# Optimization experiments

Hardware: AMD Instinct MI355X
Metric: run time of the kernel (lower is better)

The kernel has to match this reference:

```python
import jax, jax.numpy as jnp
import numpy as np

HID = 1024
HEADS = 16
HEAD_DIM = HID // HEADS
FFN = 4096
EPS = 1e-5


def setup_inputs() -> dict:
    key = jax.random.key(0)
    ks = jax.random.split(key, 12)
    s = lambda k, shape, fan_in: jax.random.normal(k, shape, jnp.float32) * (fan_in ** -0.5)
    return {
        "hidden_states": jax.random.normal(ks[0], (2, 2048, HID), jnp.float32),
        "Wq": s(ks[1], (HID, HID), HID),
        "Wk": s(ks[2], (HID, HID), HID),
        "Wv": s(ks[3], (HID, HID), HID),
        "Wo": s(ks[4], (HID, HID), HID),
        "W1": s(ks[5], (HID, FFN), HID),
        "b1": jnp.zeros((FFN,), jnp.float32),
        "W2": s(ks[6], (FFN, HID), FFN),
        "b2": jnp.zeros((HID,), jnp.float32),
        "ln1_scale": jnp.ones((HID,), jnp.float32),
        "ln1_shift": jnp.zeros((HID,), jnp.float32),
        "ln2_scale": jnp.ones((HID,), jnp.float32),
        "ln2_shift": jnp.zeros((HID,), jnp.float32),
    }


def _layer_norm(x, scale, shift):
    mean = jnp.mean(x, axis=-1, keepdims=True)
    var = jnp.var(x, axis=-1, keepdims=True)  # biased, matches unbiased=False
    return (x - mean) * jax.lax.rsqrt(var + EPS) * scale + shift


def _forward(hidden_states, Wq, Wk, Wv, Wo, W1, b1, W2, b2,
             ln1_scale, ln1_shift, ln2_scale, ln2_shift):
    bsz, seq_len, _ = hidden_states.shape
    residual = hidden_states
    x = _layer_norm(hidden_states, ln1_scale, ln1_shift)

    # q/k/v projections -> [b, h, s, d]
    def proj(W):
        return (x @ W).reshape(bsz, seq_len, HEADS, HEAD_DIM).transpose(0, 2, 1, 3)
    q, k, v = proj(Wq), proj(Wk), proj(Wv)

    scores = jnp.einsum("bhqd,bhkd->bhqk", q, k)
    causal = jnp.triu(jnp.ones((seq_len, seq_len), bool), k=1)
    scores = jnp.where(causal, -jnp.inf, scores) / (HEAD_DIM ** 0.5)
    attn = jax.nn.softmax(scores, axis=-1)  # dropout is identity in eval
    out = jnp.einsum("bhqk,bhkd->bhqd", attn, v)
    out = out.transpose(0, 2, 1, 3).reshape(bsz, seq_len, HID)
    hidden_states = residual + out @ Wo

    residual = hidden_states
    y = _layer_norm(hidden_states, ln2_scale, ln2_shift)
    y = jax.nn.gelu(y @ W1 + b1, approximate=False) @ W2 + b2  # torch nn.GELU default = exact erf
    return residual + y


def reference(hidden_states, Wq, Wk, Wv, Wo, W1, b1, W2, b2,
              ln1_scale, ln1_shift, ln2_scale, ln2_shift):
    return _forward(hidden_states, Wq, Wk, Wv, Wo, W1, b1, W2, b2,
                    ln1_scale, ln1_shift, ln2_scale, ln2_shift)
```

## Files before the change

kernel.cpp:

```cpp
#include <hip/hip_runtime.h>
#include <math.h>

using bf16x8 = __attribute__((ext_vector_type(8))) short;
using f32x4  = __attribute__((ext_vector_type(4))) float;

struct __align__(8) us4 { unsigned short x, y, z, w; };
struct __align__(8) u32x2 { unsigned int x, y; };

__device__ __forceinline__ unsigned short f2b(float f) {
  union { float f; unsigned u; } v; v.f = f;
  unsigned r = v.u + 0x7FFFu + ((v.u >> 16) & 1u);
  return (unsigned short)(r >> 16);
}
__device__ __forceinline__ unsigned int cvt_pk_bf16(float lo, float hi) {
  unsigned int d;
  asm("v_cvt_pk_bf16_f32 %0, %1, %2" : "=v"(d) : "v"(lo), "v"(hi));
  return d;
}

#define GLDS(g, l) __builtin_amdgcn_global_load_lds(                        \
    (const __attribute__((address_space(1))) void*)(g),                    \
    (__attribute__((address_space(3))) void*)(l), 16, 0, 0)

__global__ void __launch_bounds__(256) prep_kernel(
    const float* __restrict__ hs, const float* __restrict__ ln1s,
    const float* __restrict__ ln1b, unsigned short* __restrict__ xb,
    const float* __restrict__ Wq, const float* __restrict__ Wk,
    const float* __restrict__ Wv, const float* __restrict__ Wo,
    const float* __restrict__ W1, const float* __restrict__ W2,
    unsigned short* __restrict__ wqkvT, unsigned short* __restrict__ woT,
    unsigned short* __restrict__ w1T, unsigned short* __restrict__ w2T) {
  const int id = blockIdx.x;
  const int t = threadIdx.x;
  __shared__ float tile[32][33];
  __shared__ float red[8];

  if (id < 4096) {
    const int row = id;
    const float4 v = ((const float4*)(hs + (size_t)row * 1024))[t];
    float s  = v.x + v.y + v.z + v.w;
    float s2 = v.x * v.x + v.y * v.y + v.z * v.z + v.w * v.w;
#pragma unroll
    for (int off = 32; off; off >>= 1) {
      s  += __shfl_xor(s,  off);
      s2 += __shfl_xor(s2, off);
    }
    const int w = t >> 6, lane = t & 63;
    if (!lane) { red[w] = s; red[4 + w] = s2; }
    __syncthreads();
    s  = red[0] + red[1] + red[2] + red[3];
    s2 = red[4] + red[5] + red[6] + red[7];
    const float mean = s * (1.0f / 1024.0f);
    const float var  = s2 * (1.0f / 1024.0f) - mean * mean;
    const float rstd = rsqrtf(var + 1e-5f);
    const float4 sc = ((const float4*)ln1s)[t];
    const float4 sh = ((const float4*)ln1b)[t];
    us4 o;
    o.x = f2b((v.x - mean) * rstd * sc.x + sh.x);
    o.y = f2b((v.y - mean) * rstd * sc.y + sh.y);
    o.z = f2b((v.z - mean) * rstd * sc.z + sh.z);
    o.w = f2b((v.w - mean) * rstd * sc.w + sh.w);
    ((us4*)(xb + (size_t)row * 1024))[t] = o;
    return;
  }

  const float* src; unsigned short* dst; int K, N, n0, k0;
  if (id < 8192) {
    const int which = (id - 4096) >> 10, local = (id - 4096) & 1023;
    src = (which == 0) ? Wq : (which == 1) ? Wk : (which == 2) ? Wv : Wo;
    dst = (which == 3) ? woT : wqkvT + (size_t)which * 1048576;
    K = 1024; N = 1024;
    n0 = (local & 31) * 32; k0 = (local >> 5) * 32;
  } else if (id < 12288) {
    const int local = id - 8192;
    src = W1; dst = w1T; K = 1024; N = 4096;
    n0 = (local & 127) * 32; k0 = (local >> 7) * 32;
  } else {
    const int local = id - 12288;
    src = W2; dst = w2T; K = 4096; N = 1024;
    n0 = (local & 31) * 32; k0 = (local >> 5) * 32;
  }
  const int tx = t & 31, ty = t >> 5;
#pragma unroll
  for (int i = 0; i < 32; i += 8)
    tile[ty + i][tx] = src[(size_t)(k0 + ty + i) * N + n0 + tx];
  __syncthreads();
#pragma unroll
  for (int i = 0; i < 32; i += 8)
    dst[(size_t)(n0 + ty + i) * K + k0 + tx] = f2b(tile[tx][ty + i]);
}

__global__ void __launch_bounds__(256) ln_kernel(
    const float* __restrict__ in, const float* __restrict__ scale,
    const float* __restrict__ shift, unsigned short* __restrict__ out) {
  const int row = blockIdx.x, t = threadIdx.x;
  const float4 v = ((const float4*)(in + (size_t)row * 1024))[t];
  float s  = v.x + v.y + v.z + v.w;
  float s2 = v.x * v.x + v.y * v.y + v.z * v.z + v.w * v.w;
#pragma unroll
  for (int off = 32; off; off >>= 1) {
    s  += __shfl_xor(s,  off);
    s2 += __shfl_xor(s2, off);
  }
  __shared__ float red[8];
  const int w = t >> 6, lane = t & 63;
  if (!lane) { red[w] = s; red[4 + w] = s2; }
  __syncthreads();
  s  = red[0] + red[1] + red[2] + red[3];
  s2 = red[4] + red[5] + red[6] + red[7];
  const float mean = s * (1.0f / 1024.0f);
  const float var  = s2 * (1.0f / 1024.0f) - mean * mean;
  const float rstd = rsqrtf(var + 1e-5f);
  const float4 sc = ((const float4*)scale)[t];
  const float4 sh = ((const float4*)shift)[t];
  us4 o;
  o.x = f2b((v.x - mean) * rstd * sc.x + sh.x);
  o.y = f2b((v.y - mean) * rstd * sc.y + sh.y);
  o.z = f2b((v.z - mean) * rstd * sc.z + sh.z);
  o.w = f2b((v.w - mean) * rstd * sc.w + sh.w);
  ((us4*)(out + (size_t)row * 1024))[t] = o;
}

template <int MODE>
__global__ void __launch_bounds__(512, 2) gemm256(
    const unsigned short* __restrict__ A, const unsigned short* __restrict__ B,
    int K, int N, unsigned short* __restrict__ outb,
    const float* __restrict__ bias, unsigned short* __restrict__ vt) {
  __shared__ unsigned short lA[2][256 * 64];
  __shared__ unsigned short lB[2][256 * 64];
  const int t = threadIdx.x, lane = t & 63;
  const int w = t >> 6, wm = w >> 2, wn = w & 3;
  const int r16 = lane & 15, g = lane >> 4;
  const int m0 = blockIdx.x * 256, n0 = blockIdx.y * 256;

  const unsigned short* aSrc[4];
  const unsigned short* bSrc[4];
#pragma unroll
  for (int p = 0; p < 4; ++p) {
    const int ci = t + p * 512, r = ci >> 3, cs = ci & 7;
    aSrc[p] = A + (size_t)(m0 + r) * K + (cs ^ (r & 7)) * 8;
    bSrc[p] = B + (size_t)(n0 + r) * K + (cs ^ (r & 7)) * 8;
  }
  int aOff[8][2], bOff[4][2];
#pragma unroll
  for (int i = 0; i < 8; ++i)
#pragma unroll
    for (int ks = 0; ks < 2; ++ks) {
      const int m = wm * 128 + i * 16 + r16, kb = ks * 4 + g;
      aOff[i][ks] = ((m << 3) + (kb ^ (m & 7))) << 3;
    }
#pragma unroll
  for (int j = 0; j < 4; ++j)
#pragma unroll
    for (int ks = 0; ks < 2; ++ks) {
      const int n = wn * 64 + j * 16 + r16, kb = ks * 4 + g;
      bOff[j][ks] = ((n << 3) + (kb ^ (n & 7))) << 3;
    }

  auto stage = [&](int buf, int kt) {
    const int off = kt * 64;
#pragma unroll
    for (int p = 0; p < 4; ++p) {
      GLDS(aSrc[p] + off, &lA[buf][(t + p * 512) * 8]);
      GLDS(bSrc[p] + off, &lB[buf][(t + p * 512) * 8]);
    }
  };

  f32x4 acc[8][4] = {};
  const int nkt = K >> 6;
  stage(0, 0);
  for (int kt = 0; kt < nkt; ++kt) {
    const int cur = kt & 1;
    if (kt + 1 < nkt) {
      stage(cur ^ 1, kt + 1);
      asm volatile("s_waitcnt vmcnt(8)" ::: "memory");
    } else {
      asm volatile("s_waitcnt vmcnt(0)" ::: "memory");
    }
    __builtin_amdgcn_s_barrier();
    __builtin_amdgcn_sched_barrier(0);
    const unsigned short* bA = lA[cur];
    const unsigned short* bB = lB[cur];
#pragma unroll
    for (int ks = 0; ks < 2; ++ks) {
      bf16x8 af[8], bfr[4];
#pragma unroll
      for (int i = 0; i < 8; ++i) af[i] = *(const bf16x8*)&bA[aOff[i][ks]];
#pragma unroll
      for (int j = 0; j < 4; ++j) bfr[j] = *(const bf16x8*)&bB[bOff[j][ks]];
      __builtin_amdgcn_s_setprio(1);
#pragma unroll
      for (int i = 0; i < 8; ++i)
#pragma unroll
        for (int j = 0; j < 4; ++j)
          acc[i][j] = __builtin_amdgcn_mfma_f32_16x16x32_bf16(
              af[i], bfr[j], acc[i][j], 0, 0, 0);
      __builtin_amdgcn_s_setprio(0);
    }
    __builtin_amdgcn_sched_barrier(0);
    __builtin_amdgcn_s_barrier();
  }

  float bj[4];
  if constexpr (MODE == 2) {
#pragma unroll
    for (int j = 0; j < 4; ++j) bj[j] = bias[n0 + wn * 64 + j * 16 + r16];
  }
#pragma unroll
  for (int i = 0; i < 8; ++i) {
    const int row0 = m0 + wm * 128 + i * 16 + g * 4;
#pragma unroll
    for (int j = 0; j < 4; ++j) {
      const int colb = n0 + wn * 64 + j * 16;
      const int col = colb + r16;
      if constexpr (MODE == 0) {
        if (colb < 2048) {
#pragma unroll
          for (int r = 0; r < 4; ++r)
            outb[(size_t)(row0 + r) * 2048 + col] = f2b(acc[i][j][r]);
        } else {
          const int b = row0 >> 11, s0 = row0 & 2047;
          us4 pk;
          pk.x = f2b(acc[i][j][0]); pk.y = f2b(acc[i][j][1]);
          pk.z = f2b(acc[i][j][2]); pk.w = f2b(acc[i][j][3]);
          *(us4*)&vt[((size_t)b * 1024 + (col - 2048)) * 2048 + s0] = pk;
        }
      } else {
#pragma unroll
        for (int r = 0; r < 4; ++r) {
          const float x = acc[i][j][r] + bj[j];
          const float u = x * (0.7978845608028654f + 0.03567740814f * x * x);
          const float e = __builtin_amdgcn_exp2f(u * 2.885390081777927f);
          const float th = 1.0f - 2.0f * __builtin_amdgcn_rcpf(e + 1.0f);
          outb[(size_t)(row0 + r) * N + col] = f2b(0.5f * x * (1.0f + th));
        }
      }
    }
  }
}

template <int MODE, int BM>
__global__ void __launch_bounds__(256) gemm_bt(
    const unsigned short* __restrict__ A, const unsigned short* __restrict__ B,
    int K, int N,
    float* __restrict__ outf, const float* __restrict__ bias,
    const float* __restrict__ resid) {
  constexpr int WN = (BM == 128) ? 2 : 4;
  constexpr int NJ = 128 / (16 * WN);
  constexpr int ACH = BM / 32;
  __shared__ unsigned short lA[2][BM * 64];
  __shared__ unsigned short lB[2][128 * 64];
  const int t = threadIdx.x, lane = t & 63;
  const int w = t >> 6, wm = w / WN, wn = w % WN;
  const int r16 = lane & 15, g = lane >> 4;
  const int m0 = blockIdx.x * BM, n0 = blockIdx.y * 128;

  const unsigned short* aSrc[ACH];
  const unsigned short* bSrc[4];
#pragma unroll
  for (int p = 0; p < ACH; ++p) {
    const int ci = t + p * 256, m = ci >> 3, cs = ci & 7;
    aSrc[p] = A + (size_t)(m0 + m) * K + (cs ^ (m & 7)) * 8;
  }
#pragma unroll
  for (int p = 0; p < 4; ++p) {
    const int ci = t + p * 256, m = ci >> 3, cs = ci & 7;
    bSrc[p] = B + (size_t)(n0 + m) * K + (cs ^ (m & 7)) * 8;
  }

  int aOff[4][2], bOff[NJ][2];
#pragma unroll
  for (int i = 0; i < 4; ++i)
#pragma unroll
    for (int ks = 0; ks < 2; ++ks) {
      const int m = wm * 64 + i * 16 + r16, kb = ks * 4 + g;
      aOff[i][ks] = ((m << 3) + (kb ^ (m & 7))) << 3;
    }
#pragma unroll
  for (int j = 0; j < NJ; ++j)
#pragma unroll
    for (int ks = 0; ks < 2; ++ks) {
      const int n = wn * (16 * NJ) + j * 16 + r16, kb = ks * 4 + g;
      bOff[j][ks] = ((n << 3) + (kb ^ (n & 7))) << 3;
    }

  auto stage = [&](int buf, int kt) {
    const int off = kt * 64;
#pragma unroll
    for (int p = 0; p < ACH; ++p)
      GLDS(aSrc[p] + off, &lA[buf][(t + p * 256) * 8]);
#pragma unroll
    for (int p = 0; p < 4; ++p)
      GLDS(bSrc[p] + off, &lB[buf][(t + p * 256) * 8]);
  };

  f32x4 acc[4][NJ] = {};
  const int nkt = K >> 6;
  stage(0, 0);
  for (int kt = 0; kt < nkt; ++kt) {
    const int cur = kt & 1;
    if (kt + 1 < nkt) {
      stage(cur ^ 1, kt + 1);
      if constexpr (ACH == 2)
        asm volatile("s_waitcnt vmcnt(6)" ::: "memory");
      else
        asm volatile("s_waitcnt vmcnt(8)" ::: "memory");
    } else {
      asm volatile("s_waitcnt vmcnt(0)" ::: "memory");
    }
    __builtin_amdgcn_s_barrier();
    __builtin_amdgcn_sched_barrier(0);
    const unsigned short* bA = lA[cur];
    const unsigned short* bB = lB[cur];
#pragma unroll
    for (int ks = 0; ks < 2; ++ks) {
      bf16x8 af[4], bfr[NJ];
#pragma unroll
      for (int i = 0; i < 4; ++i) af[i] = *(const bf16x8*)&bA[aOff[i][ks]];
#pragma unroll
      for (int j = 0; j < NJ; ++j) bfr[j] = *(const bf16x8*)&bB[bOff[j][ks]];
      __builtin_amdgcn_s_setprio(1);
#pragma unroll
      for (int i = 0; i < 4; ++i)
#pragma unroll
        for (int j = 0; j < NJ; ++j)
          acc[i][j] = __builtin_amdgcn_mfma_f32_16x16x32_bf16(
              af[i], bfr[j], acc[i][j], 0, 0, 0);
      __builtin_amdgcn_s_setprio(0);
    }
    __builtin_amdgcn_sched_barrier(0);
    __builtin_amdgcn_s_barrier();
  }

  float bj[NJ];
  if constexpr (MODE == 3) {
#pragma unroll
    for (int j = 0; j < NJ; ++j)
      bj[j] = bias[n0 + wn * (16 * NJ) + j * 16 + r16];
  }
#pragma unroll
  for (int i = 0; i < 4; ++i) {
    const int row0 = m0 + wm * 64 + i * 16 + g * 4;
#pragma unroll
    for (int j = 0; j < NJ; ++j) {
      const int col = n0 + wn * (16 * NJ) + j * 16 + r16;
      if constexpr (MODE == 1) {
#pragma unroll
        for (int r = 0; r < 4; ++r) {
          const size_t idx = (size_t)(row0 + r) * N + col;
          outf[idx] = acc[i][j][r] + resid[idx];
        }
      } else {
#pragma unroll
        for (int r = 0; r < 4; ++r) {
          const size_t idx = (size_t)(row0 + r) * N + col;
          outf[idx] = acc[i][j][r] + bj[j] + resid[idx];
        }
      }
    }
  }
}

__global__ void __launch_bounds__(256) attn_kernel(
    const unsigned short* __restrict__ qk, const unsigned short* __restrict__ vt,
    unsigned short* __restrict__ obuf) {
  const int j = blockIdx.x, h = blockIdx.y, bb = blockIdx.z;
  const int t = threadIdx.x, lane = t & 63, w = t >> 6;
  const int r16 = lane & 15, g = lane >> 4;
  __shared__ unsigned short lK[2][64 * 64];
  __shared__ unsigned short lV[2][64 * 64];
  __shared__ unsigned short lP[4][16 * 64];

  const int qtA = j, qtB = 31 - j;
  const int ktmax = qtB;
  const int qrowA = qtA * 64 + w * 16 + r16;
  const int qrowB = qtB * 64 + w * 16 + r16;
  const float CE = 0.18033688011112042f;

  bf16x8 qfA[2], qfB[2];
  {
    const unsigned short* qa = qk + (size_t)(bb * 2048 + qrowA) * 2048 + h * 64;
    qfA[0] = *(const bf16x8*)(qa + g * 8);
    qfA[1] = *(const bf16x8*)(qa + 32 + g * 8);
    const unsigned short* qb = qk + (size_t)(bb * 2048 + qrowB) * 2048 + h * 64;
    qfB[0] = *(const bf16x8*)(qb + g * 8);
    qfB[1] = *(const bf16x8*)(qb + 32 + g * 8);
  }

  f32x4 accA[4] = {}, accB[4] = {};
  float mA = -3.0e38f, lA_ = 0.0f, mB = -3.0e38f, lB_ = 0.0f;

  auto stage = [&](int buf, int kt) {
    const int k0 = kt * 64;
#pragma unroll
    for (int p = 0; p < 2; ++p) {
      const int ci = t + p * 256;
      const int r = ci >> 3, cs = ci & 7;
      const int cb = cs ^ (r & 7);
      GLDS(qk + (size_t)(bb * 2048 + k0 + r) * 2048 + 1024 + h * 64 + cb * 8,
           &lK[buf][ci * 8]);
      GLDS(vt + ((size_t)bb * 1024 + h * 64 + r) * 2048 + k0 + cb * 8,
           &lV[buf][ci * 8]);
    }
  };

  const int pswz = (r16 & 7) << 3;

  auto flash_step = [&](const bf16x8* qf, f32x4* accO, float& mrun,
                        float& lrun, int qrow, bool diag, int k0, int cur) {
    f32x4 s[4] = {};
    __builtin_amdgcn_s_setprio(1);
#pragma unroll
    for (int ks = 0; ks < 2; ++ks)
#pragma unroll
      for (int mt = 0; mt < 4; ++mt) {
        const int r = mt * 16 + r16, db = ks * 4 + g;
        const bf16x8 kf =
            *(const bf16x8*)&lK[cur][((r << 3) + (db ^ (r & 7))) << 3];
        s[mt] = __builtin_amdgcn_mfma_f32_16x16x32_bf16(kf, qf[ks], s[mt],
                                                        0, 0, 0);
      }
    __builtin_amdgcn_s_setprio(0);
    if (diag) {
#pragma unroll
      for (int mt = 0; mt < 4; ++mt)
#pragma unroll
        for (int r = 0; r < 4; ++r)
          if (k0 + mt * 16 + g * 4 + r > qrow) s[mt][r] = -3.0e38f;
    }
    float tmax = -3.0e38f;
#pragma unroll
    for (int mt = 0; mt < 4; ++mt)
#pragma unroll
      for (int r = 0; r < 4; ++r) tmax = fmaxf(tmax, s[mt][r]);
    tmax = fmaxf(tmax, __shfl_xor(tmax, 16));
    tmax = fmaxf(tmax, __shfl_xor(tmax, 32));
    if (!__all(tmax <= mrun + 44.0f)) {
      const float mnew = fmaxf(mrun, tmax);
      const float fac = __builtin_amdgcn_exp2f((mrun - mnew) * CE);
      lrun *= fac;
      float fr[4];
#pragma unroll
      for (int r = 0; r < 4; ++r) fr[r] = __shfl(fac, g * 4 + r);
#pragma unroll
      for (int nb = 0; nb < 4; ++nb)
#pragma unroll
        for (int r = 0; r < 4; ++r) accO[nb][r] *= fr[r];
      mrun = mnew;
    }
    float pv[4][4];
    float tsum = 0.0f;
#pragma unroll
    for (int mt = 0; mt < 4; ++mt)
#pragma unroll
      for (int r = 0; r < 4; ++r) {
        pv[mt][r] = __builtin_amdgcn_exp2f((s[mt][r] - mrun) * CE);
        tsum += pv[mt][r];
      }
    tsum += __shfl_xor(tsum, 16);
    tsum += __shfl_xor(tsum, 32);
    lrun += tsum;
#pragma unroll
    for (int mt = 0; mt < 4; ++mt) {
      u32x2 pk;
      pk.x = cvt_pk_bf16(pv[mt][0], pv[mt][1]);
      pk.y = cvt_pk_bf16(pv[mt][2], pv[mt][3]);
      *(u32x2*)&lP[w][r16 * 64 + ((mt * 16 + g * 4) ^ pswz)] = pk;
    }
    __builtin_amdgcn_s_setprio(1);
#pragma unroll
    for (int ks = 0; ks < 2; ++ks) {
      const bf16x8 pa =
          *(const bf16x8*)&lP[w][r16 * 64 + ((ks * 32 + g * 8) ^ pswz)];
#pragma unroll
      for (int nb = 0; nb < 4; ++nb) {
        const int d = nb * 16 + r16, kb = ks * 4 + g;
        const bf16x8 vf =
            *(const bf16x8*)&lV[cur][((d << 3) + (kb ^ (d & 7))) << 3];
        accO[nb] = __builtin_amdgcn_mfma_f32_16x16x32_bf16(pa, vf, accO[nb],
                                                           0, 0, 0);
      }
    }
    __builtin_amdgcn_s_setprio(0);
  };

  stage(0, 0);
  __syncthreads();
  int cur = 0;
  for (int kt = 0; kt <= ktmax; ++kt) {
    if (kt < ktmax) stage(cur ^ 1, kt + 1);
    flash_step(qfB, accB, mB, lB_, qrowB, kt == qtB, kt * 64, cur);
    if (kt <= qtA)
      flash_step(qfA, accA, mA, lA_, qrowA, kt == qtA, kt * 64, cur);
    __syncthreads();
    cur ^= 1;
  }

  auto epilogue = [&](const f32x4* accO, float lrun, int q0) {
    const float li = 1.0f / lrun;
    float lr_[4];
#pragma unroll
    for (int r = 0; r < 4; ++r) lr_[r] = __shfl(li, g * 4 + r);
#pragma unroll
    for (int nb = 0; nb < 4; ++nb)
#pragma unroll
      for (int r = 0; r < 4; ++r) {
        const int row = bb * 2048 + q0 + w * 16 + g * 4 + r;
        const int col = h * 64 + nb * 16 + r16;
        obuf[(size_t)row * 1024 + col] = f2b(accO[nb][r] * lr_[r]);
      }
  };
  epilogue(accA, lA_, qtA * 64);
  epilogue(accB, lB_, qtB * 64);
}

extern "C" void kernel_launch(void* const* d_in, const int* in_sizes, int n_in,
                              void* d_out, int out_size, void* d_ws,
                              size_t ws_size, hipStream_t stream) {
  const float* hs   = (const float*)d_in[0];
  const float* Wq   = (const float*)d_in[1];
  const float* Wk   = (const float*)d_in[2];
  const float* Wv   = (const float*)d_in[3];
  const float* Wo   = (const float*)d_in[4];
  const float* W1   = (const float*)d_in[5];
  const float* b1   = (const float*)d_in[6];
  const float* W2   = (const float*)d_in[7];
  const float* b2   = (const float*)d_in[8];
  const float* ln1s = (const float*)d_in[9];
  const float* ln1b = (const float*)d_in[10];
  const float* ln2s = (const float*)d_in[11];
  const float* ln2b = (const float*)d_in[12];
  float* out = (float*)d_out;

  char* ws = (char*)d_ws;
  unsigned short* wqkvT = (unsigned short*)(ws + 0);
  unsigned short* woT   = (unsigned short*)(ws + 6291456);
  unsigned short* w1T   = (unsigned short*)(ws + 8388608);
  unsigned short* w2T   = (unsigned short*)(ws + 16777216);
  float*          hid   = (float*)(ws + 25165824);
  unsigned short* xb    = (unsigned short*)(ws + 41943040);
  char*           big   = ws + 50331648;
  unsigned short* qkb   = (unsigned short*)(big);
  unsigned short* vtb   = (unsigned short*)(big + 16777216);
  unsigned short* ob    = (unsigned short*)(big + 25165824);
  unsigned short* h1    = (unsigned short*)(big);

  prep_kernel<<<16384, 256, 0, stream>>>(hs, ln1s, ln1b, xb,
                                         Wq, Wk, Wv, Wo, W1, W2,
                                         wqkvT, woT, w1T, w2T);
  gemm256<0><<<dim3(16, 12), 512, 0, stream>>>(xb, wqkvT, 1024, 3072,
                                               qkb, nullptr, vtb);
  attn_kernel<<<dim3(16, 16, 2), 256, 0, stream>>>(qkb, vtb, ob);
  gemm_bt<1, 64><<<dim3(64, 8), 256, 0, stream>>>(ob, woT, 1024, 1024,
                                                  hid, nullptr, hs);
  ln_kernel<<<4096, 256, 0, stream>>>(hid, ln2s, ln2b, xb);
  gemm256<2><<<dim3(16, 16), 512, 0, stream>>>(xb, w1T, 1024, 4096,
                                               h1, b1, nullptr);
  gemm_bt<3, 64><<<dim3(64, 8), 256, 0, stream>>>(h1, w2T, 4096, 1024,
                                                  out, b2, hid);
}
```

Before: 229.9 us.

## Replace 256x256 double-buffered GEMM with 128x128 single-buffer tiles

The QKV and FFN1 GEMMs now use a 128x128 tile, 256-thread kernel with a single LDS buffer and plain __syncthreads, replacing the 256x256, 512-thread, double-buffered kernel that used explicit vmcnt waits. Grids grow from 192/256 blocks to 768/1024, which fills the 256 CUs more evenly and cuts LDS use per block so more blocks can be resident. In exchange, global loads no longer overlap MFMA work inside a block, and the smaller tiles reuse each loaded element less.

```diff
diff --git a/kernel.cpp b/kernel.cpp
--- a/kernel.cpp
+++ b/kernel.cpp
@@ -122,83 +122,64 @@
 }
 
 template <int MODE>
-__global__ void __launch_bounds__(512, 2) gemm256(
+__global__ void __launch_bounds__(256) gemm_sb(
     const unsigned short* __restrict__ A, const unsigned short* __restrict__ B,
     int K, int N, unsigned short* __restrict__ outb,
     const float* __restrict__ bias, unsigned short* __restrict__ vt) {
-  __shared__ unsigned short lA[2][256 * 64];
-  __shared__ unsigned short lB[2][256 * 64];
+  __shared__ unsigned short lA[128 * 64];
+  __shared__ unsigned short lB[128 * 64];
   const int t = threadIdx.x, lane = t & 63;
-  const int w = t >> 6, wm = w >> 2, wn = w & 3;
+  const int w = t >> 6, wm = w >> 1, wn = w & 1;
   const int r16 = lane & 15, g = lane >> 4;
-  const int m0 = blockIdx.x * 256, n0 = blockIdx.y * 256;
+  const int m0 = blockIdx.x * 128, n0 = blockIdx.y * 128;
 
   const unsigned short* aSrc[4];
   const unsigned short* bSrc[4];
 #pragma unroll
   for (int p = 0; p < 4; ++p) {
-    const int ci = t + p * 512, r = ci >> 3, cs = ci & 7;
-    aSrc[p] = A + (size_t)(m0 + r) * K + (cs ^ (r & 7)) * 8;
-    bSrc[p] = B + (size_t)(n0 + r) * K + (cs ^ (r & 7)) * 8;
-  }
-  int aOff[8][2], bOff[4][2];
-#pragma unroll
-  for (int i = 0; i < 8; ++i)
+    const int ci = t + p * 256, m = ci >> 3, cs = ci & 7;
+    aSrc[p] = A + (size_t)(m0 + m) * K + (cs ^ (m & 7)) * 8;
+    bSrc[p] = B + (size_t)(n0 + m) * K + (cs ^ (m & 7)) * 8;
+  }
+  int aOff[4][2], bOff[4][2];
+#pragma unroll
+  for (int i = 0; i < 4; ++i)
 #pragma unroll
     for (int ks = 0; ks < 2; ++ks) {
-      const int m = wm * 128 + i * 16 + r16, kb = ks * 4 + g;
+      const int m = wm * 64 + i * 16 + r16, kb = ks * 4 + g;
       aOff[i][ks] = ((m << 3) + (kb ^ (m & 7))) << 3;
-    }
-#pragma unroll
-  for (int j = 0; j < 4; ++j)
+      const int n = wn * 64 + i * 16 + r16;
+      bOff[i][ks] = ((n << 3) + (kb ^ (n & 7))) << 3;
+    }
+
+  f32x4 acc[4][4] = {};
+  const int nkt = K >> 6;
+  for (int kt = 0; kt < nkt; ++kt) {
+    if (kt) __syncthreads();
+    const int off = kt * 64;
+#pragma unroll
+    for (int p = 0; p < 4; ++p) {
+      GLDS(aSrc[p] + off, &lA[(t + p * 256) * 8]);
+      GLDS(bSrc[p] + off, &lB[(t + p * 256) * 8]);
+    }
+    __syncthreads();
 #pragma unroll
     for (int ks = 0; ks < 2; ++ks) {
-      const int n = wn * 64 + j * 16 + r16, kb = ks * 4 + g;
-      bOff[j][ks] = ((n << 3) + (kb ^ (n & 7))) << 3;
-    }
-
-  auto stage = [&](int buf, int kt) {
-    const int off = kt * 64;
-#pragma unroll
-    for (int p = 0; p < 4; ++p) {
-      GLDS(aSrc[p] + off, &lA[buf][(t + p * 512) * 8]);
-      GLDS(bSrc[p] + off, &lB[buf][(t + p * 512) * 8]);
-    }
-  };
-
-  f32x4 acc[8][4] = {};
-  const int nkt = K >> 6;
-  stage(0, 0);
-  for (int kt = 0; kt < nkt; ++kt) {
-    const int cur = kt & 1;
-    if (kt + 1 < nkt) {
-      stage(cur ^ 1, kt + 1);
-      asm volatile("s_waitcnt vmcnt(8)" ::: "memory");
-    } else {
-      asm volatile("s_waitcnt vmcnt(0)" ::: "memory");
-    }
-    __builtin_amdgcn_s_barrier();
-    __builtin_amdgcn_sched_barrier(0);
-    const unsigned short* bA = lA[cur];
-    const unsigned short* bB = lB[cur];
-#pragma unroll
-    for (int ks = 0; ks < 2; ++ks) {
-      bf16x8 af[8], bfr[4];
-#pragma unroll
-      for (int i = 0; i < 8; ++i) af[i] = *(const bf16x8*)&bA[aOff[i][ks]];
-#pragma unroll
-      for (int j = 0; j < 4; ++j) bfr[j] = *(const bf16x8*)&bB[bOff[j][ks]];
+      bf16x8 af[4], bfr[4];
+#pragma unroll
+      for (int i = 0; i < 4; ++i) {
+        af[i]  = *(const bf16x8*)&lA[aOff[i][ks]];
+        bfr[i] = *(const bf16x8*)&lB[bOff[i][ks]];
+      }
       __builtin_amdgcn_s_setprio(1);
 #pragma unroll
-      for (int i = 0; i < 8; ++i)
+      for (int i = 0; i < 4; ++i)
 #pragma unroll
         for (int j = 0; j < 4; ++j)
           acc[i][j] = __builtin_amdgcn_mfma_f32_16x16x32_bf16(
               af[i], bfr[j], acc[i][j], 0, 0, 0);
       __builtin_amdgcn_s_setprio(0);
     }
-    __builtin_amdgcn_sched_barrier(0);
-    __builtin_amdgcn_s_barrier();
   }
 
   float bj[4];
@@ -207,8 +188,8 @@
     for (int j = 0; j < 4; ++j) bj[j] = bias[n0 + wn * 64 + j * 16 + r16];
   }
 #pragma unroll
-  for (int i = 0; i < 8; ++i) {
-    const int row0 = m0 + wm * 128 + i * 16 + g * 4;
+  for (int i = 0; i < 4; ++i) {
+    const int row0 = m0 + wm * 64 + i * 16 + g * 4;
 #pragma unroll
     for (int j = 0; j < 4; ++j) {
       const int colb = n0 + wn * 64 + j * 16;
@@ -548,13 +529,13 @@
   prep_kernel<<<16384, 256, 0, stream>>>(hs, ln1s, ln1b, xb,
                                          Wq, Wk, Wv, Wo, W1, W2,
                                          wqkvT, woT, w1T, w2T);
-  gemm256<0><<<dim3(16, 12), 512, 0, stream>>>(xb, wqkvT, 1024, 3072,
+  gemm_sb<0><<<dim3(32, 24), 256, 0, stream>>>(xb, wqkvT, 1024, 3072,
                                                qkb, nullptr, vtb);
   attn_kernel<<<dim3(16, 16, 2), 256, 0, stream>>>(qkb, vtb, ob);
   gemm_bt<1, 64><<<dim3(64, 8), 256, 0, stream>>>(ob, woT, 1024, 1024,
                                                   hid, nullptr, hs);
   ln_kernel<<<4096, 256, 0, stream>>>(hid, ln2s, ln2b, xb);
-  gemm256<2><<<dim3(16, 16), 512, 0, stream>>>(xb, w1T, 1024, 4096,
+  gemm_sb<2><<<dim3(32, 32), 256, 0, stream>>>(xb, w1T, 1024, 4096,
                                                h1, b1, nullptr);
   gemm_bt<3, 64><<<dim3(64, 8), 256, 0, stream>>>(h1, w2T, 4096, 1024,
                                                   out, b2, hid);
```

Result: no change. 229.6 us (-0.1%).

## Restructure 256x256 GEMM into 8-phase ping-pong pipeline with half-tile staging

Applied to the files above, without the earlier changes.

Replaces the double-buffered 256x256 GEMM main loop with an 8-phase schedule. Each K-step is split into four MFMA quadrants, and loads of A and B half-tiles for future iterations are interleaved between them, so global-to-LDS copies, LDS reads and MFMAs overlap at finer granularity. The warp-to-tile mapping is changed to interleaved rows and columns, with matching epilogue indices. This adds more barriers and hand-tuned vmcnt/lgkmcnt waits, which could be fragile or stall if the counts are off.

```diff
diff --git a/kernel.cpp b/kernel.cpp
--- a/kernel.cpp
+++ b/kernel.cpp
@@ -122,7 +122,7 @@
 }
 
 template <int MODE>
-__global__ void __launch_bounds__(512, 2) gemm256(
+__global__ void __launch_bounds__(512, 2) gemm8p(
     const unsigned short* __restrict__ A, const unsigned short* __restrict__ B,
     int K, int N, unsigned short* __restrict__ outb,
     const float* __restrict__ bias, unsigned short* __restrict__ vt) {
@@ -133,85 +133,167 @@
   const int r16 = lane & 15, g = lane >> 4;
   const int m0 = blockIdx.x * 256, n0 = blockIdx.y * 256;
 
-  const unsigned short* aSrc[4];
-  const unsigned short* bSrc[4];
-#pragma unroll
-  for (int p = 0; p < 4; ++p) {
+  const unsigned short* aS[2];
+  const unsigned short* bS[2];
+  int ldst[2];
+#pragma unroll
+  for (int p = 0; p < 2; ++p) {
     const int ci = t + p * 512, r = ci >> 3, cs = ci & 7;
-    aSrc[p] = A + (size_t)(m0 + r) * K + (cs ^ (r & 7)) * 8;
-    bSrc[p] = B + (size_t)(n0 + r) * K + (cs ^ (r & 7)) * 8;
-  }
+    aS[p] = A + (size_t)(m0 + r) * K + (cs ^ (r & 7)) * 8;
+    bS[p] = B + (size_t)(n0 + r) * K + (cs ^ (r & 7)) * 8;
+    ldst[p] = ci * 8;
+  }
+  const size_t hstep = (size_t)128 * K;
+
+  auto stageA = [&](int buf, int kt, int half) {
+    const size_t off = (size_t)kt * 64 + (half ? hstep : 0);
+    const int dof = half ? 8192 : 0;
+#pragma unroll
+    for (int p = 0; p < 2; ++p) GLDS(aS[p] + off, &lA[buf][dof + ldst[p]]);
+  };
+  auto stageB = [&](int buf, int kt, int half) {
+    const size_t off = (size_t)kt * 64 + (half ? hstep : 0);
+    const int dof = half ? 8192 : 0;
+#pragma unroll
+    for (int p = 0; p < 2; ++p) GLDS(bS[p] + off, &lB[buf][dof + ldst[p]]);
+  };
+
   int aOff[8][2], bOff[4][2];
 #pragma unroll
   for (int i = 0; i < 8; ++i)
 #pragma unroll
     for (int ks = 0; ks < 2; ++ks) {
-      const int m = wm * 128 + i * 16 + r16, kb = ks * 4 + g;
-      aOff[i][ks] = ((m << 3) + (kb ^ (m & 7))) << 3;
+      const int row = i * 32 + wm * 16 + r16, kb = ks * 4 + g;
+      aOff[i][ks] = ((row << 3) + (kb ^ (row & 7))) << 3;
     }
 #pragma unroll
   for (int j = 0; j < 4; ++j)
 #pragma unroll
     for (int ks = 0; ks < 2; ++ks) {
-      const int n = wn * 64 + j * 16 + r16, kb = ks * 4 + g;
-      bOff[j][ks] = ((n << 3) + (kb ^ (n & 7))) << 3;
-    }
-
-  auto stage = [&](int buf, int kt) {
-    const int off = kt * 64;
-#pragma unroll
-    for (int p = 0; p < 4; ++p) {
-      GLDS(aSrc[p] + off, &lA[buf][(t + p * 512) * 8]);
-      GLDS(bSrc[p] + off, &lB[buf][(t + p * 512) * 8]);
-    }
+      const int row = j * 64 + wn * 16 + r16, kb = ks * 4 + g;
+      bOff[j][ks] = ((row << 3) + (kb ^ (row & 7))) << 3;
+    }
+
+  auto vwait = [](int n) {
+    if (n >= 10)     asm volatile("s_waitcnt vmcnt(10)" ::: "memory");
+    else if (n >= 8) asm volatile("s_waitcnt vmcnt(8)" ::: "memory");
+    else if (n >= 4) asm volatile("s_waitcnt vmcnt(4)" ::: "memory");
+    else if (n >= 2) asm volatile("s_waitcnt vmcnt(2)" ::: "memory");
+    else             asm volatile("s_waitcnt vmcnt(0)" ::: "memory");
   };
 
+  const int nkt = K >> 6;
+  stageA(0, 0, 0); stageB(0, 0, 0); stageB(0, 0, 1); stageA(0, 0, 1);
+  stageA(1, 1, 0); stageB(1, 1, 0); stageB(1, 1, 1);
+  asm volatile("s_waitcnt vmcnt(10)" ::: "memory");
+  __builtin_amdgcn_s_barrier();
+
   f32x4 acc[8][4] = {};
-  const int nkt = K >> 6;
-  stage(0, 0);
+  bf16x8 af[4][2], b01[2][2], b23[2][2];
   for (int kt = 0; kt < nkt; ++kt) {
-    const int cur = kt & 1;
-    if (kt + 1 < nkt) {
-      stage(cur ^ 1, kt + 1);
-      asm volatile("s_waitcnt vmcnt(8)" ::: "memory");
-    } else {
-      asm volatile("s_waitcnt vmcnt(0)" ::: "memory");
-    }
-    __builtin_amdgcn_s_barrier();
-    __builtin_amdgcn_sched_barrier(0);
+    const int cur = kt & 1, nxt = cur ^ 1;
     const unsigned short* bA = lA[cur];
     const unsigned short* bB = lB[cur];
 #pragma unroll
-    for (int ks = 0; ks < 2; ++ks) {
-      bf16x8 af[8], bfr[4];
-#pragma unroll
-      for (int i = 0; i < 8; ++i) af[i] = *(const bf16x8*)&bA[aOff[i][ks]];
-#pragma unroll
-      for (int j = 0; j < 4; ++j) bfr[j] = *(const bf16x8*)&bB[bOff[j][ks]];
-      __builtin_amdgcn_s_setprio(1);
-#pragma unroll
-      for (int i = 0; i < 8; ++i)
-#pragma unroll
-        for (int j = 0; j < 4; ++j)
-          acc[i][j] = __builtin_amdgcn_mfma_f32_16x16x32_bf16(
-              af[i], bfr[j], acc[i][j], 0, 0, 0);
-      __builtin_amdgcn_s_setprio(0);
-    }
+    for (int i = 0; i < 4; ++i) {
+      af[i][0] = *(const bf16x8*)&bA[aOff[i][0]];
+      af[i][1] = *(const bf16x8*)&bA[aOff[i][1]];
+    }
+#pragma unroll
+    for (int j = 0; j < 2; ++j) {
+      b01[j][0] = *(const bf16x8*)&bB[bOff[j][0]];
+      b01[j][1] = *(const bf16x8*)&bB[bOff[j][1]];
+    }
+    if (kt + 1 < nkt) stageA(nxt, kt + 1, 1);
+    asm volatile("s_waitcnt lgkmcnt(8)" ::: "memory");
+    vwait(kt == nkt - 1 ? 2 : 10);
+    __builtin_amdgcn_s_barrier();
+    asm volatile("s_waitcnt lgkmcnt(0)" ::: "memory");
     __builtin_amdgcn_sched_barrier(0);
+    __builtin_amdgcn_s_setprio(1);
+#pragma unroll
+    for (int i = 0; i < 4; ++i)
+#pragma unroll
+      for (int j = 0; j < 2; ++j) {
+        acc[i][j] = __builtin_amdgcn_mfma_f32_16x16x32_bf16(
+            af[i][0], b01[j][0], acc[i][j], 0, 0, 0);
+        acc[i][j] = __builtin_amdgcn_mfma_f32_16x16x32_bf16(
+            af[i][1], b01[j][1], acc[i][j], 0, 0, 0);
+      }
+    __builtin_amdgcn_s_setprio(0);
+    __builtin_amdgcn_s_barrier();
+#pragma unroll
+    for (int j = 0; j < 2; ++j) {
+      b23[j][0] = *(const bf16x8*)&bB[bOff[2 + j][0]];
+      b23[j][1] = *(const bf16x8*)&bB[bOff[2 + j][1]];
+    }
+    if (kt + 2 < nkt) stageB(cur, kt + 2, 0);
+    vwait(kt == nkt - 1 ? 0 : (kt == nkt - 2 ? 8 : 10));
+    __builtin_amdgcn_s_barrier();
+    asm volatile("s_waitcnt lgkmcnt(0)" ::: "memory");
+    __builtin_amdgcn_sched_barrier(0);
+    __builtin_amdgcn_s_setprio(1);
+#pragma unroll
+    for (int i = 0; i < 4; ++i)
+#pragma unroll
+      for (int j = 0; j < 2; ++j) {
+        acc[i][2 + j] = __builtin_amdgcn_mfma_f32_16x16x32_bf16(
+            af[i][0], b23[j][0], acc[i][2 + j], 0, 0, 0);
+        acc[i][2 + j] = __builtin_amdgcn_mfma_f32_16x16x32_bf16(
+            af[i][1], b23[j][1], acc[i][2 + j], 0, 0, 0);
+      }
+    __builtin_amdgcn_s_setprio(0);
+    __builtin_amdgcn_s_barrier();
+#pragma unroll
+    for (int i = 0; i < 4; ++i) {
+      af[i][0] = *(const bf16x8*)&bA[aOff[4 + i][0]];
+      af[i][1] = *(const bf16x8*)&bA[aOff[4 + i][1]];
+    }
+    if (kt + 2 < nkt) stageA(cur, kt + 2, 0);
+    __builtin_amdgcn_s_barrier();
+    asm volatile("s_waitcnt lgkmcnt(0)" ::: "memory");
+    __builtin_amdgcn_sched_barrier(0);
+    __builtin_amdgcn_s_setprio(1);
+#pragma unroll
+    for (int i = 0; i < 4; ++i)
+#pragma unroll
+      for (int j = 0; j < 2; ++j) {
+        acc[4 + i][j] = __builtin_amdgcn_mfma_f32_16x16x32_bf16(
+            af[i][0], b01[j][0], acc[4 + i][j], 0, 0, 0);
+        acc[4 + i][j] = __builtin_amdgcn_mfma_f32_16x16x32_bf16(
+            af[i][1], b01[j][1], acc[4 + i][j], 0, 0, 0);
+      }
+    __builtin_amdgcn_s_setprio(0);
+    __builtin_amdgcn_s_barrier();
+    if (kt + 2 < nkt) stageB(cur, kt + 2, 1);
+    __builtin_amdgcn_s_barrier();
+    __builtin_amdgcn_s_setprio(1);
+#pragma unroll
+    for (int i = 0; i < 4; ++i)
+#pragma unroll
+      for (int j = 0; j < 2; ++j) {
+        acc[4 + i][2 + j] = __builtin_amdgcn_mfma_f32_16x16x32_bf16(
+            af[i][0], b23[j][0], acc[4 + i][2 + j], 0, 0, 0);
+        acc[4 + i][2 + j] = __builtin_amdgcn_mfma_f32_16x16x32_bf16(
+            af[i][1], b23[j][1], acc[4 + i][2 + j], 0, 0, 0);
+      }
+    __builtin_amdgcn_s_setprio(0);
+    if (kt < nkt - 1) vwait(kt == nkt - 2 ? 4 : 10);
     __builtin_amdgcn_s_barrier();
   }
 
   float bj[4];
   if constexpr (MODE == 2) {
 #pragma unroll
-    for (int j = 0; j < 4; ++j) bj[j] = bias[n0 + wn * 64 + j * 16 + r16];
+    for (int j = 0; j < 4; ++j)
+      bj[j] = bias[n0 + j * 64 + wn * 16 + r16];
   }
 #pragma unroll
   for (int i = 0; i < 8; ++i) {
-    const int row0 = m0 + wm * 128 + i * 16 + g * 4;
+    const int row0 = m0 + i * 32 + wm * 16 + g * 4;
 #pragma unroll
     for (int j = 0; j < 4; ++j) {
-      const int colb = n0 + wn * 64 + j * 16;
+      const int colb = n0 + j * 64 + wn * 16;
       const int col = colb + r16;
       if constexpr (MODE == 0) {
         if (colb < 2048) {
@@ -548,14 +630,14 @@
   prep_kernel<<<16384, 256, 0, stream>>>(hs, ln1s, ln1b, xb,
                                          Wq, Wk, Wv, Wo, W1, W2,
                                          wqkvT, woT, w1T, w2T);
-  gemm256<0><<<dim3(16, 12), 512, 0, stream>>>(xb, wqkvT, 1024, 3072,
-                                               qkb, nullptr, vtb);
+  gemm8p<0><<<dim3(16, 12), 512, 0, stream>>>(xb, wqkvT, 1024, 3072,
+                                              qkb, nullptr, vtb);
   attn_kernel<<<dim3(16, 16, 2), 256, 0, stream>>>(qkb, vtb, ob);
   gemm_bt<1, 64><<<dim3(64, 8), 256, 0, stream>>>(ob, woT, 1024, 1024,
                                                   hid, nullptr, hs);
   ln_kernel<<<4096, 256, 0, stream>>>(hid, ln2s, ln2b, xb);
-  gemm256<2><<<dim3(16, 16), 512, 0, stream>>>(xb, w1T, 1024, 4096,
-                                               h1, b1, nullptr);
+  gemm8p<2><<<dim3(16, 16), 512, 0, stream>>>(xb, w1T, 1024, 4096,
+                                              h1, b1, nullptr);
   gemm_bt<3, 64><<<dim3(64, 8), 256, 0, stream>>>(h1, w2T, 4096, 1024,
                                                   out, b2, hid);
 }
```

Result: faster. 224.5 us (-2.4%).
